# Optimization experiments

Measured on AMD Instinct MI355X. Metric: run time of the kernel, lower is better.

The kernel has to match this reference:

```python
import jax, jax.numpy as jnp
import numpy as np

D = 1024      # in_features
H = 4096      # hidden_dims
E = 8         # expert_nums
K = 2         # top_k
B, S = 4, 2048


def setup_inputs() -> dict:
    key = jax.random.key(0)
    ks = jax.random.split(key, 8)
    def lin(k, fan_in, shape):
        bound = 1.0 / np.sqrt(fan_in)
        return jax.random.uniform(k, shape, jnp.float32, -bound, bound)
    return {
        "x":  jax.random.normal(ks[0], (B, S, D), jnp.float32),
        "Wg": lin(ks[1], D, (D, E)),
        "bg": lin(ks[2], D, (E,)),
        "W1": lin(ks[3], D, (E, D, H)),
        "b1": lin(ks[4], D, (E, H)),
        "W2": lin(ks[5], H, (E, H, D)),
        "b2": lin(ks[6], H, (E, D)),
    }


def reference(x, Wg, bg, W1, b1, W2, b2):
    B_, S_, D_ = x.shape
    xt = x.reshape(-1, D_)                                   # [N, D]
    # Router: softmax gating + top-k
    logits = xt @ Wg + bg                                    # [N, E]
    scores = jax.nn.softmax(logits, axis=-1)
    topk_probs, topk_idx = jax.lax.top_k(scores, K)          # [N, K]
    # Dense per-expert FFN (the source runs every expert on all tokens)
    h = jnp.einsum("nd,edh->enh", xt, W1) + b1[:, None, :]   # [E, N, H]
    h = jax.nn.gelu(h, approximate=False)
    eo = jnp.einsum("enh,ehd->end", h, W2) + b2[:, None, :]  # [E, N, D]
    # Gather selected experts per token and combine with gate weights
    eo = jnp.transpose(eo, (1, 0, 2))                        # [N, E, D]
    sel = jnp.take_along_axis(eo, topk_idx[:, :, None], axis=1)  # [N, K, D]
    out = jnp.einsum("nk,nkd->nd", topk_probs, sel)          # [N, D]
    return out.reshape(B_, S_, D_)
```

## Files before the change

### kernel.cpp

```cpp
#include <hip/hip_runtime.h>
#include <hip/hip_bf16.h>
#include <cstdint>
#include <cstddef>

using bf16 = __hip_bfloat16;
using short8 = __attribute__((ext_vector_type(8))) short;
using floatx4 = __attribute__((ext_vector_type(4))) float;

constexpr int D_IN = 1024;
constexpr int H_DIM = 4096;
constexpr int E_NUM = 8;
constexpr int NTOK = 8192;
constexpr int NPAIR = NTOK * 2;
constexpr int MAXT = 136;

constexpr size_t OFF_PTOK  = 1024;
constexpr size_t OFF_PPROB = 263168;
constexpr size_t OFF_SCHED = 525312;
constexpr size_t OFF_XBF   = 1048576;
constexpr size_t OFF_W2T   = OFF_XBF + (size_t)NTOK * D_IN * 2;
constexpr size_t OFF_HBUF  = OFF_W2T + (size_t)E_NUM * D_IN * H_DIM * 2;
constexpr size_t OFF_W1T   = OFF_HBUF + (size_t)NPAIR * H_DIM * 2;

__device__ __forceinline__ void cp16(const bf16* g, bf16* s) {
  __builtin_amdgcn_global_load_lds(
      (const __attribute__((address_space(1))) unsigned int*)g,
      (__attribute__((address_space(3))) unsigned int*)s, 16, 0, 0);
}

__global__ __launch_bounds__(256) void transpose_cvt(
    const float* __restrict__ in, bf16* __restrict__ out, int K, int N) {
  __shared__ float tile[64][65];
  const int e = blockIdx.z;
  const float* ip = in + (size_t)e * K * N + (size_t)(blockIdx.y * 64) * N + blockIdx.x * 64;
  bf16* op = out + (size_t)e * K * N + (size_t)(blockIdx.x * 64) * K + blockIdx.y * 64;
  const int tc = threadIdx.x & 15;
  const int tr = threadIdx.x >> 4;
#pragma unroll
  for (int r = 0; r < 4; r++) {
    const float4 v = *(const float4*)&ip[(size_t)(tr + r * 16) * N + tc * 4];
    *(float4*)&tile[tr + r * 16][tc * 4] = v;
  }
  __syncthreads();
  const int kg = threadIdx.x & 7;
  const int nb = threadIdx.x >> 3;
#pragma unroll
  for (int r = 0; r < 2; r++) {
    const int n = nb + r * 32;
    union { short8 v; bf16 h[8]; } u;
#pragma unroll
    for (int j = 0; j < 8; j++) u.h[j] = __float2bfloat16(tile[kg * 8 + j][n]);
    *(short8*)&op[(size_t)n * K + kg * 8] = u.v;
  }
}

__global__ __launch_bounds__(256) void router_kernel(
    const float* __restrict__ x, const float* __restrict__ Wg,
    const float* __restrict__ bg, bf16* __restrict__ Xbf,
    int* __restrict__ counts, int* __restrict__ pairTok, float* __restrict__ pairProb) {
  __shared__ int lcnt[E_NUM];
  __shared__ int sBase[E_NUM];
  __shared__ int sE0[32], sL0[32], sE1[32], sL1[32];
  __shared__ float sP0[32], sP1[32];
  const int lane = threadIdx.x & 63;
  const int wave = threadIdx.x >> 6;
  if (threadIdx.x < E_NUM) lcnt[threadIdx.x] = 0;
  __syncthreads();

  for (int tk = 0; tk < 8; tk++) {
    const int li = wave * 8 + tk;
    const int n = blockIdx.x * 32 + li;
    const float* xr = x + (size_t)n * D_IN;
    bf16* xbr = Xbf + (size_t)n * D_IN;
    float logit[E_NUM];
#pragma unroll
    for (int e = 0; e < E_NUM; e++) logit[e] = 0.f;
#pragma unroll
    for (int i = 0; i < 16; i++) {
      const int d = i * 64 + lane;
      const float xd = xr[d];
      xbr[d] = __float2bfloat16(xd);
      const float4* wr = (const float4*)(Wg + (size_t)d * E_NUM);
      const float4 w0 = wr[0], w1 = wr[1];
      logit[0] += xd * w0.x; logit[1] += xd * w0.y;
      logit[2] += xd * w0.z; logit[3] += xd * w0.w;
      logit[4] += xd * w1.x; logit[5] += xd * w1.y;
      logit[6] += xd * w1.z; logit[7] += xd * w1.w;
    }
#pragma unroll
    for (int e = 0; e < E_NUM; e++) {
#pragma unroll
      for (int off = 32; off >= 1; off >>= 1)
        logit[e] += __shfl_xor(logit[e], off, 64);
    }
    if (lane == 0) {
      float l[E_NUM], mx = -1e30f;
#pragma unroll
      for (int e = 0; e < E_NUM; e++) { l[e] = logit[e] + bg[e]; mx = fmaxf(mx, l[e]); }
      float ex[E_NUM], s = 0.f;
#pragma unroll
      for (int e = 0; e < E_NUM; e++) { ex[e] = expf(l[e] - mx); s += ex[e]; }
      int i0 = 0;
#pragma unroll
      for (int e = 1; e < E_NUM; e++) if (l[e] > l[i0]) i0 = e;
      int i1 = (i0 == 0) ? 1 : 0;
#pragma unroll
      for (int e = 0; e < E_NUM; e++) if (e != i0 && l[e] > l[i1]) i1 = e;
      const float inv = 1.f / s;
      sE0[li] = i0; sL0[li] = atomicAdd(&lcnt[i0], 1); sP0[li] = ex[i0] * inv;
      sE1[li] = i1; sL1[li] = atomicAdd(&lcnt[i1], 1); sP1[li] = ex[i1] * inv;
    }
  }
  __syncthreads();
  if (threadIdx.x < E_NUM)
    sBase[threadIdx.x] = atomicAdd(&counts[threadIdx.x], lcnt[threadIdx.x]);
  __syncthreads();
  if (threadIdx.x < 32) {
    const int li = threadIdx.x;
    const int n = blockIdx.x * 32 + li;
    const int e0 = sE0[li], p0 = sBase[e0] + sL0[li];
    pairTok[e0 * NTOK + p0] = n;
    pairProb[e0 * NTOK + p0] = sP0[li];
    const int e1 = sE1[li], p1 = sBase[e1] + sL1[li];
    pairTok[e1 * NTOK + p1] = n | (1 << 15);
    pairProb[e1 * NTOK + p1] = sP1[li];
  }
}

__global__ void sched_kernel(const int* __restrict__ counts, int* __restrict__ sched) {
  if (threadIdx.x == 0 && blockIdx.x == 0) {
    int* bases = sched;
    int* nTiles = sched + 8;
    int* tileMap = sched + 16;
    int base = 0, t = 0;
    for (int e = 0; e < E_NUM; e++) {
      bases[e] = base;
      const int nt = (counts[e] + 127) >> 7;
      for (int m = 0; m < nt; m++) tileMap[t++] = (e << 16) | m;
      base += counts[e];
    }
    *nTiles = t;
  }
}

template <int MODE, int K, int NC, int KS>
__global__ __launch_bounds__(256, 3) void gemm_kernel(
    const bf16* __restrict__ A, const bf16* __restrict__ Wt,
    const float* __restrict__ bias, const int* __restrict__ counts,
    const int* __restrict__ pairTok, const float* __restrict__ pairProb,
    const int* __restrict__ sched, bf16* __restrict__ Hout, float* __restrict__ out) {
  const int tix = blockIdx.x % MAXT;
  int nb = blockIdx.x / MAXT;
  if (tix >= sched[8]) return;
  int ks = 0;
  if (MODE == 1) { ks = nb >> 3; nb &= 7; }
  constexpr int KJOB = K / KS;
  constexpr int NT = KJOB / 32;
  const int ksOff = ks * KJOB;

  const int packed = sched[16 + tix];
  const int e = packed >> 16;
  const int m0 = (packed & 0xFFFF) * 128;
  const int cnt = counts[e];
  const int base = sched[e];
  const int n0 = nb * 128;

  __shared__ __align__(16) bf16 As[3 * 128 * 32];
  __shared__ __align__(16) bf16 Bs[3 * 128 * 32];

  const int t = threadIdx.x;
  const int lane = t & 63;
  const int wave = t >> 6;
  const int wm = wave >> 1, wn = wave & 1;
  const int fr = lane & 15;
  const int csel = ((lane >> 4) ^ (lane & 3)) << 3;
  const int aBase = (wm * 64 + fr) * 32 + csel;
  const int bBase = (wn * 64 + fr) * 32 + csel;

  const int r0 = t >> 2, r1 = 64 + (t >> 2);
  const int gc = (((t & 3) ^ (r0 & 3)) << 3);
  int p0 = m0 + r0; if (p0 > cnt - 1) p0 = cnt - 1;
  int p1 = m0 + r1; if (p1 > cnt - 1) p1 = cnt - 1;
  const bf16 *aS0, *aS1;
  if (MODE == 0) {
    aS0 = A + (size_t)(pairTok[e * NTOK + p0] & 0x1FFF) * K + gc;
    aS1 = A + (size_t)(pairTok[e * NTOK + p1] & 0x1FFF) * K + gc;
  } else {
    aS0 = A + (size_t)(base + p0) * K + ksOff + gc;
    aS1 = A + (size_t)(base + p1) * K + ksOff + gc;
  }
  const bf16* bS0 = Wt + ((size_t)e * NC + n0 + r0) * K + ksOff + gc;
  const bf16* bS1 = Wt + ((size_t)e * NC + n0 + r1) * K + ksOff + gc;

  floatx4 acc[4][4];
#pragma unroll
  for (int ti = 0; ti < 4; ti++)
#pragma unroll
    for (int tj = 0; tj < 4; tj++)
      acc[ti][tj] = {0.f, 0.f, 0.f, 0.f};

#pragma unroll
  for (int q = 0; q < 3; q++) {
    cp16(aS0 + q * 32, &As[q * 4096 + t * 8]);
    cp16(aS1 + q * 32, &As[q * 4096 + 2048 + t * 8]);
    cp16(bS0 + q * 32, &Bs[q * 4096 + t * 8]);
    cp16(bS1 + q * 32, &Bs[q * 4096 + 2048 + t * 8]);
  }
  asm volatile("s_waitcnt vmcnt(8)" ::: "memory");
  __builtin_amdgcn_sched_barrier(0);
  __builtin_amdgcn_s_barrier();
  __builtin_amdgcn_sched_barrier(0);

  int rb = 0;
#pragma unroll 1
  for (int kt = 0; kt < NT; kt++) {
    short8 a[4], b[4];
#pragma unroll
    for (int i = 0; i < 4; i++) {
      a[i] = *(const short8*)&As[rb + aBase + i * 512];
      b[i] = *(const short8*)&Bs[rb + bBase + i * 512];
    }
    asm volatile("s_waitcnt lgkmcnt(0)" ::: "memory");
    __builtin_amdgcn_sched_barrier(0);
    __builtin_amdgcn_s_barrier();
    __builtin_amdgcn_sched_barrier(0);
    const int kq = (kt + 3) * 32;
    cp16(aS0 + kq, &As[rb + t * 8]);
    cp16(aS1 + kq, &As[rb + 2048 + t * 8]);
    cp16(bS0 + kq, &Bs[rb + t * 8]);
    cp16(bS1 + kq, &Bs[rb + 2048 + t * 8]);
    __builtin_amdgcn_s_setprio(1);
#pragma unroll
    for (int ti = 0; ti < 4; ti++)
#pragma unroll
      for (int tj = 0; tj < 4; tj++)
        acc[ti][tj] = __builtin_amdgcn_mfma_f32_16x16x32_bf16(a[ti], b[tj], acc[ti][tj], 0, 0, 0);
    __builtin_amdgcn_s_setprio(0);
    asm volatile("s_waitcnt vmcnt(8)" ::: "memory");
    __builtin_amdgcn_sched_barrier(0);
    __builtin_amdgcn_s_barrier();
    __builtin_amdgcn_sched_barrier(0);
    rb += 4096;
    if (rb == 12288) rb = 0;
  }

  float bv[4];
#pragma unroll
  for (int tj = 0; tj < 4; tj++)
    bv[tj] = bias[(size_t)e * NC + n0 + wn * 64 + tj * 16 + fr];

#pragma unroll
  for (int ti = 0; ti < 4; ti++) {
    const int rbrow = wm * 64 + ti * 16 + (lane >> 4) * 4;
#pragma unroll
    for (int i = 0; i < 4; i++) {
      const int p = m0 + rbrow + i;
      if (p < cnt) {
        if (MODE == 0) {
          bf16* orow = Hout + (size_t)(base + p) * NC + n0 + wn * 64 + fr;
#pragma unroll
          for (int tj = 0; tj < 4; tj++) {
            const float h = acc[ti][tj][i] + bv[tj];
            const float g = 0.5f * h * (1.f + erff(h * 0.70710678118f));
            orow[tj * 16] = __float2bfloat16(g);
          }
        } else {
          const int pt = pairTok[e * NTOK + p];
          const float pr = pairProb[e * NTOK + p];
          const int tok = pt & 0x1FFF;
          float* orow = out + (size_t)tok * NC + n0 + wn * 64 + fr;
#pragma unroll
          for (int tj = 0; tj < 4; tj++) {
            float v = acc[ti][tj][i];
            if (ks == 0) v += bv[tj];
            atomicAdd(&orow[tj * 16], v * pr);
          }
        }
      }
    }
  }
}

extern "C" void kernel_launch(void* const* d_in, const int* in_sizes, int n_in,
                              void* d_out, int out_size, void* d_ws, size_t ws_size,
                              hipStream_t stream) {
  const float* x  = (const float*)d_in[0];
  const float* Wg = (const float*)d_in[1];
  const float* bg = (const float*)d_in[2];
  const float* W1 = (const float*)d_in[3];
  const float* b1 = (const float*)d_in[4];
  const float* W2 = (const float*)d_in[5];
  const float* b2 = (const float*)d_in[6];
  float* out = (float*)d_out;
  char* ws = (char*)d_ws;

  int*   counts   = (int*)ws;
  int*   pairTok  = (int*)(ws + OFF_PTOK);
  float* pairProb = (float*)(ws + OFF_PPROB);
  int*   sched    = (int*)(ws + OFF_SCHED);
  bf16*  Xbf      = (bf16*)(ws + OFF_XBF);
  bf16*  W2t      = (bf16*)(ws + OFF_W2T);
  bf16*  Hbuf     = (bf16*)(ws + OFF_HBUF);
  bf16*  W1t      = (bf16*)(ws + OFF_W1T);

  hipMemsetAsync(counts, 0, 64, stream);
  hipMemsetAsync(out, 0, (size_t)NTOK * D_IN * sizeof(float), stream);
  transpose_cvt<<<dim3(H_DIM / 64, D_IN / 64, E_NUM), 256, 0, stream>>>(W1, W1t, D_IN, H_DIM);
  transpose_cvt<<<dim3(D_IN / 64, H_DIM / 64, E_NUM), 256, 0, stream>>>(W2, W2t, H_DIM, D_IN);
  router_kernel<<<NTOK / 32, 256, 0, stream>>>(x, Wg, bg, Xbf, counts, pairTok, pairProb);
  sched_kernel<<<1, 64, 0, stream>>>(counts, sched);
  gemm_kernel<0, D_IN, H_DIM, 1><<<32 * MAXT, 256, 0, stream>>>(
      Xbf, W1t, b1, counts, pairTok, pairProb, sched, Hbuf, nullptr);
  gemm_kernel<1, H_DIM, D_IN, 2><<<16 * MAXT, 256, 0, stream>>>(
      Hbuf, W2t, b2, counts, pairTok, pairProb, sched, nullptr, out);
}
```

Measured before the change: 884.8 us.

## Remap GEMM blocks per XCD, software-pipeline LDS reads, drop LDS swizzle

Block indices are remapped so that each XCD handles contiguous supertiles of (token tile, column block) pairs, with the aim of improving L2 reuse of weights and activations within a chiplet. The main loop is restructured so that LDS fragments for the next k-step are loaded while the MFMAs for the current step run, using double-buffered registers and one barrier per step. Prefetch indices are clamped at the end instead of running past the buffer. The XOR swizzle on LDS placement is removed, which may bring back LDS bank conflicts.

After: 821.2 us. -7.2%, faster.

```diff
diff --git a/kernel.cpp b/kernel.cpp
--- a/kernel.cpp
+++ b/kernel.cpp
@@ -149,13 +149,26 @@
     const float* __restrict__ bias, const int* __restrict__ counts,
     const int* __restrict__ pairTok, const float* __restrict__ pairProb,
     const int* __restrict__ sched, bf16* __restrict__ Hout, float* __restrict__ out) {
-  const int tix = blockIdx.x % MAXT;
-  int nb = blockIdx.x / MAXT;
-  if (tix >= sched[8]) return;
-  int ks = 0;
-  if (MODE == 1) { ks = nb >> 3; nb &= 7; }
   constexpr int KJOB = K / KS;
   constexpr int NT = KJOB / 32;
+
+  const int xcd = blockIdx.x & 7;
+  const int loc = blockIdx.x >> 3;
+  const int sg  = loc >> 5;
+  const int j   = loc & 31;
+  int tix, nb, ks = 0;
+  if (MODE == 0) {
+    const int st = xcd * 17 + sg;
+    tix = (st >> 2) * 4 + (j >> 3);
+    nb  = (st & 3) * 8 + (j & 7);
+  } else {
+    const int st = xcd * 9 + sg;
+    if (st >= 68) return;
+    ks  = st >= 34 ? 1 : 0;
+    tix = (st - ks * 34) * 4 + (j >> 3);
+    nb  = j & 7;
+  }
+  if (tix >= sched[8]) return;
   const int ksOff = ks * KJOB;
 
   const int packed = sched[16 + tix];
@@ -173,12 +186,12 @@
   const int wave = t >> 6;
   const int wm = wave >> 1, wn = wave & 1;
   const int fr = lane & 15;
-  const int csel = ((lane >> 4) ^ (lane & 3)) << 3;
-  const int aBase = (wm * 64 + fr) * 32 + csel;
-  const int bBase = (wn * 64 + fr) * 32 + csel;
+  const int kg = (lane >> 4) << 3;
+  const int aBase = (wm * 64 + fr) * 32 + kg;
+  const int bBase = (wn * 64 + fr) * 32 + kg;
 
   const int r0 = t >> 2, r1 = 64 + (t >> 2);
-  const int gc = (((t & 3) ^ (r0 & 3)) << 3);
+  const int gc = (t & 3) << 3;
   int p0 = m0 + r0; if (p0 > cnt - 1) p0 = cnt - 1;
   int p1 = m0 + r1; if (p1 > cnt - 1) p1 = cnt - 1;
   const bf16 *aS0, *aS1;
@@ -211,37 +224,46 @@
   __builtin_amdgcn_s_barrier();
   __builtin_amdgcn_sched_barrier(0);
 
-  int rb = 0;
-#pragma unroll 1
-  for (int kt = 0; kt < NT; kt++) {
-    short8 a[4], b[4];
-#pragma unroll
-    for (int i = 0; i < 4; i++) {
-      a[i] = *(const short8*)&As[rb + aBase + i * 512];
-      b[i] = *(const short8*)&Bs[rb + bBase + i * 512];
-    }
-    asm volatile("s_waitcnt lgkmcnt(0)" ::: "memory");
+  short8 aC[4], bC[4], aN[4], bN[4];
+#pragma unroll
+  for (int i = 0; i < 4; i++) {
+    aC[i] = *(const short8*)&As[aBase + i * 512];
+    bC[i] = *(const short8*)&Bs[bBase + i * 512];
+  }
+
+  auto step = [&](int kt, int rbW, int rbR, short8 (&ac)[4], short8 (&bc)[4],
+                  short8 (&an)[4], short8 (&bn)[4]) {
+    asm volatile("s_waitcnt vmcnt(4) lgkmcnt(0)" ::: "memory");
     __builtin_amdgcn_sched_barrier(0);
     __builtin_amdgcn_s_barrier();
     __builtin_amdgcn_sched_barrier(0);
-    const int kq = (kt + 3) * 32;
-    cp16(aS0 + kq, &As[rb + t * 8]);
-    cp16(aS1 + kq, &As[rb + 2048 + t * 8]);
-    cp16(bS0 + kq, &Bs[rb + t * 8]);
-    cp16(bS1 + kq, &Bs[rb + 2048 + t * 8]);
+    int kq = (kt + 3) * 32;
+    if (kq > KJOB - 32) kq = KJOB - 32;
+    cp16(aS0 + kq, &As[rbW + t * 8]);
+    cp16(aS1 + kq, &As[rbW + 2048 + t * 8]);
+    cp16(bS0 + kq, &Bs[rbW + t * 8]);
+    cp16(bS1 + kq, &Bs[rbW + 2048 + t * 8]);
+#pragma unroll
+    for (int i = 0; i < 4; i++) {
+      an[i] = *(const short8*)&As[rbR + aBase + i * 512];
+      bn[i] = *(const short8*)&Bs[rbR + bBase + i * 512];
+    }
     __builtin_amdgcn_s_setprio(1);
 #pragma unroll
     for (int ti = 0; ti < 4; ti++)
 #pragma unroll
       for (int tj = 0; tj < 4; tj++)
-        acc[ti][tj] = __builtin_amdgcn_mfma_f32_16x16x32_bf16(a[ti], b[tj], acc[ti][tj], 0, 0, 0);
+        acc[ti][tj] = __builtin_amdgcn_mfma_f32_16x16x32_bf16(ac[ti], bc[tj], acc[ti][tj], 0, 0, 0);
     __builtin_amdgcn_s_setprio(0);
-    asm volatile("s_waitcnt vmcnt(8)" ::: "memory");
-    __builtin_amdgcn_sched_barrier(0);
-    __builtin_amdgcn_s_barrier();
-    __builtin_amdgcn_sched_barrier(0);
-    rb += 4096;
-    if (rb == 12288) rb = 0;
+  };
+
+  int rbW = 0, rbR = 4096;
+#pragma unroll 1
+  for (int kt = 0; kt < NT; kt += 2) {
+    step(kt, rbW, rbR, aC, bC, aN, bN);
+    rbW = rbR; rbR += 4096; if (rbR == 12288) rbR = 0;
+    step(kt + 1, rbW, rbR, aN, bN, aC, bC);
+    rbW = rbR; rbR += 4096; if (rbR == 12288) rbR = 0;
   }
 
   float bv[4];
@@ -309,8 +331,8 @@
   transpose_cvt<<<dim3(D_IN / 64, H_DIM / 64, E_NUM), 256, 0, stream>>>(W2, W2t, H_DIM, D_IN);
   router_kernel<<<NTOK / 32, 256, 0, stream>>>(x, Wg, bg, Xbf, counts, pairTok, pairProb);
   sched_kernel<<<1, 64, 0, stream>>>(counts, sched);
-  gemm_kernel<0, D_IN, H_DIM, 1><<<32 * MAXT, 256, 0, stream>>>(
+  gemm_kernel<0, D_IN, H_DIM, 1><<<8 * 17 * 32, 256, 0, stream>>>(
       Xbf, W1t, b1, counts, pairTok, pairProb, sched, Hbuf, nullptr);
-  gemm_kernel<1, H_DIM, D_IN, 2><<<16 * MAXT, 256, 0, stream>>>(
+  gemm_kernel<1, H_DIM, D_IN, 2><<<8 * 9 * 32, 256, 0, stream>>>(
       Hbuf, W2t, b2, counts, pairTok, pairProb, sched, nullptr, out);
 }
```

## Switch grouped expert GEMMs to 256x256 tiles with 8 waves and XCD-aware mapping

Applied to the files above, without the earlier changes.

Replaces the 128x128, 4-wave grouped GEMM with a 256x256 tile, 8-wave kernel using K-step 64, double-buffered LDS (128KB), and a four-phase interleave of LDS reads, async global-to-LDS loads and MFMA quadrants. Block indices are remapped so that blocks sharing an expert tile land on the same XCD, and the scheduler now emits 256-row tiles. The goal is higher arithmetic intensity and better L2 reuse per XCD. The cost is more padding waste on partial expert tiles and lower occupancy from the large LDS and register footprint. The hard-coded grid mapping assumes at most 36 (MODE 0) or 18 (MODE 1) tiles.

New measurement: 848.5 us. -4.1%, faster.

```diff
diff --git a/kernel.cpp b/kernel.cpp
--- a/kernel.cpp
+++ b/kernel.cpp
@@ -12,7 +12,6 @@
 constexpr int E_NUM = 8;
 constexpr int NTOK = 8192;
 constexpr int NPAIR = NTOK * 2;
-constexpr int MAXT = 136;
 
 constexpr size_t OFF_PTOK  = 1024;
 constexpr size_t OFF_PPROB = 263168;
@@ -27,6 +26,10 @@
       (const __attribute__((address_space(1))) unsigned int*)g,
       (__attribute__((address_space(3))) unsigned int*)s, 16, 0, 0);
 }
+
+#define SCB() __builtin_amdgcn_sched_barrier(0)
+#define BARRIER() { __builtin_amdgcn_s_barrier(); SCB(); }
+#define LGKM0() { asm volatile("s_waitcnt lgkmcnt(0)" ::: "memory"); SCB(); }
 
 __global__ __launch_bounds__(256) void transpose_cvt(
     const float* __restrict__ in, bf16* __restrict__ out, int K, int N) {
@@ -135,7 +138,7 @@
     int base = 0, t = 0;
     for (int e = 0; e < E_NUM; e++) {
       bases[e] = base;
-      const int nt = (counts[e] + 127) >> 7;
+      const int nt = (counts[e] + 255) >> 8;
       for (int m = 0; m < nt; m++) tileMap[t++] = (e << 16) | m;
       base += counts[e];
     }
@@ -144,141 +147,209 @@
 }
 
 template <int MODE, int K, int NC, int KS>
-__global__ __launch_bounds__(256, 3) void gemm_kernel(
+__global__ __launch_bounds__(512, 2) void gemm8(
     const bf16* __restrict__ A, const bf16* __restrict__ Wt,
     const float* __restrict__ bias, const int* __restrict__ counts,
     const int* __restrict__ pairTok, const float* __restrict__ pairProb,
     const int* __restrict__ sched, bf16* __restrict__ Hout, float* __restrict__ out) {
-  const int tix = blockIdx.x % MAXT;
-  int nb = blockIdx.x / MAXT;
-  if (tix >= sched[8]) return;
-  int ks = 0;
-  if (MODE == 1) { ks = nb >> 3; nb &= 7; }
   constexpr int KJOB = K / KS;
-  constexpr int NT = KJOB / 32;
+  constexpr int NT = KJOB / 64;
+
+  __shared__ __align__(16) bf16 L[65536];
+
+  const int xcd = blockIdx.x & 7;
+  const int q = blockIdx.x >> 3;
+  const int sg = q >> 5;
+  const int j = q & 31;
+  int mt, nb, ks = 0;
+  if (MODE == 0) {
+    const int st = xcd * 5 + sg;
+    if (st >= 36) return;
+    mt = (st >> 1) * 4 + (j >> 3);
+    nb = (st & 1) * 8 + (j & 7);
+  } else {
+    const int st = xcd * 3 + sg;
+    if (st >= 18) return;
+    ks = st >= 9 ? 1 : 0;
+    mt = (st - ks * 9) * 8 + (j >> 2);
+    nb = j & 3;
+  }
+  if (mt >= sched[8]) return;
   const int ksOff = ks * KJOB;
 
-  const int packed = sched[16 + tix];
+  const int packed = sched[16 + mt];
   const int e = packed >> 16;
-  const int m0 = (packed & 0xFFFF) * 128;
+  const int m0 = (packed & 0xFFFF) * 256;
   const int cnt = counts[e];
   const int base = sched[e];
-  const int n0 = nb * 128;
-
-  __shared__ __align__(16) bf16 As[3 * 128 * 32];
-  __shared__ __align__(16) bf16 Bs[3 * 128 * 32];
-
-  const int t = threadIdx.x;
-  const int lane = t & 63;
-  const int wave = t >> 6;
-  const int wm = wave >> 1, wn = wave & 1;
+  const int n0 = nb * 256;
+
+  const int tid = threadIdx.x;
+  const int lane = tid & 63;
+  const int wave = tid >> 6;
+  const int wm = wave >> 2, wn = wave & 3;
   const int fr = lane & 15;
-  const int csel = ((lane >> 4) ^ (lane & 3)) << 3;
-  const int aBase = (wm * 64 + fr) * 32 + csel;
-  const int bBase = (wn * 64 + fr) * 32 + csel;
-
-  const int r0 = t >> 2, r1 = 64 + (t >> 2);
-  const int gc = (((t & 3) ^ (r0 & 3)) << 3);
-  int p0 = m0 + r0; if (p0 > cnt - 1) p0 = cnt - 1;
-  int p1 = m0 + r1; if (p1 > cnt - 1) p1 = cnt - 1;
-  const bf16 *aS0, *aS1;
-  if (MODE == 0) {
-    aS0 = A + (size_t)(pairTok[e * NTOK + p0] & 0x1FFF) * K + gc;
-    aS1 = A + (size_t)(pairTok[e * NTOK + p1] & 0x1FFF) * K + gc;
-  } else {
-    aS0 = A + (size_t)(base + p0) * K + ksOff + gc;
-    aS1 = A + (size_t)(base + p1) * K + ksOff + gc;
-  }
-  const bf16* bS0 = Wt + ((size_t)e * NC + n0 + r0) * K + ksOff + gc;
-  const bf16* bS1 = Wt + ((size_t)e * NC + n0 + r1) * K + ksOff + gc;
-
-  floatx4 acc[4][4];
-#pragma unroll
-  for (int ti = 0; ti < 4; ti++)
-#pragma unroll
-    for (int tj = 0; tj < 4; tj++)
-      acc[ti][tj] = {0.f, 0.f, 0.f, 0.f};
-
-#pragma unroll
-  for (int q = 0; q < 3; q++) {
-    cp16(aS0 + q * 32, &As[q * 4096 + t * 8]);
-    cp16(aS1 + q * 32, &As[q * 4096 + 2048 + t * 8]);
-    cp16(bS0 + q * 32, &Bs[q * 4096 + t * 8]);
-    cp16(bS1 + q * 32, &Bs[q * 4096 + 2048 + t * 8]);
-  }
-  asm volatile("s_waitcnt vmcnt(8)" ::: "memory");
-  __builtin_amdgcn_sched_barrier(0);
-  __builtin_amdgcn_s_barrier();
-  __builtin_amdgcn_sched_barrier(0);
-
-  int rb = 0;
+  const int g = lane >> 4;
+
+  const int r = tid >> 3;
+  const int cg8 = (((tid & 7) ^ (r & 7)) << 3);
+  const bf16* aP[4];
+  const bf16* bP[4];
+#pragma unroll
+  for (int i = 0; i < 4; i++) {
+    const int rr = r + i * 64;
+    int p = m0 + rr; if (p > cnt - 1) p = cnt - 1;
+    if (MODE == 0) {
+      aP[i] = A + (size_t)(pairTok[e * NTOK + p] & 0x1FFF) * K + cg8;
+    } else {
+      aP[i] = A + (size_t)(base + p) * K + ksOff + cg8;
+    }
+    bP[i] = Wt + ((size_t)e * NC + n0 + rr) * K + ksOff + cg8;
+  }
+
+  int aOff[2], bOff[2];
+#pragma unroll
+  for (int ksl = 0; ksl < 2; ksl++) {
+    const int c = (g + ksl * 4) ^ (lane & 7);
+    aOff[ksl] = (wm * 128 + fr) * 64 + c * 8;
+    bOff[ksl] = 16384 + (wn * 64 + fr) * 64 + c * 8;
+  }
+
+  floatx4 acc[8][4];
+#pragma unroll
+  for (int mi = 0; mi < 8; mi++)
+#pragma unroll
+    for (int nf = 0; nf < 4; nf++) acc[mi][nf] = {0.f, 0.f, 0.f, 0.f};
+
+  auto stageA = [&](int half, int t, int bufS) {
+    const int kq = (t < NT ? t : NT - 1) * 64;
+    cp16(aP[half * 2 + 0] + kq, &L[bufS + half * 8192 + tid * 8]);
+    cp16(aP[half * 2 + 1] + kq, &L[bufS + half * 8192 + 4096 + tid * 8]);
+  };
+  auto stageB = [&](int half, int t, int bufS) {
+    const int kq = (t < NT ? t : NT - 1) * 64;
+    cp16(bP[half * 2 + 0] + kq, &L[bufS + 16384 + half * 8192 + tid * 8]);
+    cp16(bP[half * 2 + 1] + kq, &L[bufS + 16384 + half * 8192 + 4096 + tid * 8]);
+  };
+
+  stageA(0, 0, 0); stageA(1, 0, 0); stageB(0, 0, 0); stageB(1, 0, 0);
+  stageA(0, 1, 32768);
+
+  short8 aR[4][2], bR[4][2];
+  int bufR = 0;
 #pragma unroll 1
-  for (int kt = 0; kt < NT; kt++) {
-    short8 a[4], b[4];
-#pragma unroll
-    for (int i = 0; i < 4; i++) {
-      a[i] = *(const short8*)&As[rb + aBase + i * 512];
-      b[i] = *(const short8*)&Bs[rb + bBase + i * 512];
-    }
-    asm volatile("s_waitcnt lgkmcnt(0)" ::: "memory");
-    __builtin_amdgcn_sched_barrier(0);
-    __builtin_amdgcn_s_barrier();
-    __builtin_amdgcn_sched_barrier(0);
-    const int kq = (kt + 3) * 32;
-    cp16(aS0 + kq, &As[rb + t * 8]);
-    cp16(aS1 + kq, &As[rb + 2048 + t * 8]);
-    cp16(bS0 + kq, &Bs[rb + t * 8]);
-    cp16(bS1 + kq, &Bs[rb + 2048 + t * 8]);
+  for (int t = 0; t < NT; ++t) {
+    const int bufS = 32768 - bufR;
+    asm volatile("s_waitcnt vmcnt(2)" ::: "memory");
+    SCB();
+    BARRIER();
+#pragma unroll
+    for (int ksl = 0; ksl < 2; ksl++) {
+#pragma unroll
+      for (int mf = 0; mf < 4; mf++)
+        aR[mf][ksl] = *(const short8*)&L[bufR + aOff[ksl] + mf * 1024];
+#pragma unroll
+      for (int nf = 0; nf < 2; nf++)
+        bR[nf][ksl] = *(const short8*)&L[bufR + bOff[ksl] + nf * 1024];
+    }
+    stageA(1, t + 1, bufS);
+    LGKM0();
     __builtin_amdgcn_s_setprio(1);
 #pragma unroll
-    for (int ti = 0; ti < 4; ti++)
-#pragma unroll
-      for (int tj = 0; tj < 4; tj++)
-        acc[ti][tj] = __builtin_amdgcn_mfma_f32_16x16x32_bf16(a[ti], b[tj], acc[ti][tj], 0, 0, 0);
+    for (int ksl = 0; ksl < 2; ksl++)
+#pragma unroll
+      for (int mf = 0; mf < 4; mf++)
+#pragma unroll
+        for (int nf = 0; nf < 2; nf++)
+          acc[mf][nf] = __builtin_amdgcn_mfma_f32_16x16x32_bf16(aR[mf][ksl], bR[nf][ksl], acc[mf][nf], 0, 0, 0);
     __builtin_amdgcn_s_setprio(0);
-    asm volatile("s_waitcnt vmcnt(8)" ::: "memory");
-    __builtin_amdgcn_sched_barrier(0);
-    __builtin_amdgcn_s_barrier();
-    __builtin_amdgcn_sched_barrier(0);
-    rb += 4096;
-    if (rb == 12288) rb = 0;
-  }
+    BARRIER();
+#pragma unroll
+    for (int ksl = 0; ksl < 2; ksl++)
+#pragma unroll
+      for (int nf = 0; nf < 2; nf++)
+        bR[2 + nf][ksl] = *(const short8*)&L[bufR + bOff[ksl] + (2 + nf) * 1024];
+    stageB(0, t + 1, bufS);
+    LGKM0();
+    __builtin_amdgcn_s_setprio(1);
+#pragma unroll
+    for (int ksl = 0; ksl < 2; ksl++)
+#pragma unroll
+      for (int mf = 0; mf < 4; mf++)
+#pragma unroll
+        for (int nf = 0; nf < 2; nf++)
+          acc[mf][2 + nf] = __builtin_amdgcn_mfma_f32_16x16x32_bf16(aR[mf][ksl], bR[2 + nf][ksl], acc[mf][2 + nf], 0, 0, 0);
+    __builtin_amdgcn_s_setprio(0);
+    BARRIER();
+#pragma unroll
+    for (int ksl = 0; ksl < 2; ksl++)
+#pragma unroll
+      for (int mf = 0; mf < 4; mf++)
+        aR[mf][ksl] = *(const short8*)&L[bufR + aOff[ksl] + 4096 + mf * 1024];
+    stageB(1, t + 1, bufS);
+    LGKM0();
+    __builtin_amdgcn_s_setprio(1);
+#pragma unroll
+    for (int ksl = 0; ksl < 2; ksl++)
+#pragma unroll
+      for (int mf = 0; mf < 4; mf++)
+#pragma unroll
+        for (int nf = 0; nf < 2; nf++)
+          acc[4 + mf][2 + nf] = __builtin_amdgcn_mfma_f32_16x16x32_bf16(aR[mf][ksl], bR[2 + nf][ksl], acc[4 + mf][2 + nf], 0, 0, 0);
+    __builtin_amdgcn_s_setprio(0);
+    BARRIER();
+    stageA(0, t + 2, bufR);
+    __builtin_amdgcn_s_setprio(1);
+#pragma unroll
+    for (int ksl = 0; ksl < 2; ksl++)
+#pragma unroll
+      for (int mf = 0; mf < 4; mf++)
+#pragma unroll
+        for (int nf = 0; nf < 2; nf++)
+          acc[4 + mf][nf] = __builtin_amdgcn_mfma_f32_16x16x32_bf16(aR[mf][ksl], bR[nf][ksl], acc[4 + mf][nf], 0, 0, 0);
+    __builtin_amdgcn_s_setprio(0);
+    bufR = bufS;
+  }
+  asm volatile("s_waitcnt vmcnt(0)" ::: "memory");
+  SCB();
 
   float bv[4];
 #pragma unroll
-  for (int tj = 0; tj < 4; tj++)
-    bv[tj] = bias[(size_t)e * NC + n0 + wn * 64 + tj * 16 + fr];
-
-#pragma unroll
-  for (int ti = 0; ti < 4; ti++) {
-    const int rbrow = wm * 64 + ti * 16 + (lane >> 4) * 4;
-#pragma unroll
-    for (int i = 0; i < 4; i++) {
-      const int p = m0 + rbrow + i;
-      if (p < cnt) {
-        if (MODE == 0) {
-          bf16* orow = Hout + (size_t)(base + p) * NC + n0 + wn * 64 + fr;
-#pragma unroll
-          for (int tj = 0; tj < 4; tj++) {
-            const float h = acc[ti][tj][i] + bv[tj];
-            const float g = 0.5f * h * (1.f + erff(h * 0.70710678118f));
-            orow[tj * 16] = __float2bfloat16(g);
-          }
-        } else {
-          const int pt = pairTok[e * NTOK + p];
-          const float pr = pairProb[e * NTOK + p];
-          const int tok = pt & 0x1FFF;
-          float* orow = out + (size_t)tok * NC + n0 + wn * 64 + fr;
-#pragma unroll
-          for (int tj = 0; tj < 4; tj++) {
-            float v = acc[ti][tj][i];
-            if (ks == 0) v += bv[tj];
-            atomicAdd(&orow[tj * 16], v * pr);
+  for (int nf = 0; nf < 4; nf++)
+    bv[nf] = bias[(size_t)e * NC + n0 + wn * 64 + nf * 16 + fr];
+
+#pragma unroll
+  for (int mq = 0; mq < 2; mq++)
+#pragma unroll
+    for (int mf = 0; mf < 4; mf++) {
+      const int rowb = m0 + wm * 128 + mq * 64 + mf * 16 + g * 4;
+#pragma unroll
+      for (int i = 0; i < 4; i++) {
+        const int p = rowb + i;
+        if (p < cnt) {
+          if (MODE == 0) {
+            bf16* orow = Hout + (size_t)(base + p) * NC + n0 + wn * 64 + fr;
+#pragma unroll
+            for (int nf = 0; nf < 4; nf++) {
+              const float h = acc[mq * 4 + mf][nf][i] + bv[nf];
+              const float gl = 0.5f * h * (1.f + erff(h * 0.70710678118f));
+              orow[nf * 16] = __float2bfloat16(gl);
+            }
+          } else {
+            const int pt = pairTok[e * NTOK + p];
+            const float pr = pairProb[e * NTOK + p];
+            const int tok = pt & 0x1FFF;
+            float* orow = out + (size_t)tok * NC + n0 + wn * 64 + fr;
+#pragma unroll
+            for (int nf = 0; nf < 4; nf++) {
+              float v = acc[mq * 4 + mf][nf][i];
+              if (ks == 0) v += bv[nf];
+              atomicAdd(&orow[nf * 16], v * pr);
+            }
           }
         }
       }
     }
-  }
 }
 
 extern "C" void kernel_launch(void* const* d_in, const int* in_sizes, int n_in,
@@ -309,8 +380,8 @@
   transpose_cvt<<<dim3(D_IN / 64, H_DIM / 64, E_NUM), 256, 0, stream>>>(W2, W2t, H_DIM, D_IN);
   router_kernel<<<NTOK / 32, 256, 0, stream>>>(x, Wg, bg, Xbf, counts, pairTok, pairProb);
   sched_kernel<<<1, 64, 0, stream>>>(counts, sched);
-  gemm_kernel<0, D_IN, H_DIM, 1><<<32 * MAXT, 256, 0, stream>>>(
+  gemm8<0, D_IN, H_DIM, 1><<<8 * 5 * 32, 512, 0, stream>>>(
       Xbf, W1t, b1, counts, pairTok, pairProb, sched, Hbuf, nullptr);
-  gemm_kernel<1, H_DIM, D_IN, 2><<<16 * MAXT, 256, 0, stream>>>(
+  gemm8<1, H_DIM, D_IN, 2><<<8 * 3 * 32, 512, 0, stream>>>(
       Hbuf, W2t, b2, counts, pairTok, pairProb, sched, nullptr, out);
 }
```
